# Optimization experiments

Measured on AMD Instinct MI355X. Metric: run time of the kernel, lower is better.

## Reference

```python
import jax, jax.numpy as jnp
import numpy as np

N, M, C, CSKIP, K = 16384, 4096, 256, 128, 3
BIG = 1e10  # distance penalty for cross-batch pairs


def setup_inputs() -> dict:
    key = jax.random.key(0)
    ks = jax.random.split(key, 6)
    return {
        "x": jax.random.normal(ks[0], (M, C), jnp.float32),
        "pos": jax.random.normal(ks[1], (M, 3), jnp.float32),
        "batch": jnp.zeros((M,), jnp.int32),
        "x_skip": jax.random.normal(ks[2], (N, CSKIP), jnp.float32),
        "pos_skip": jax.random.normal(ks[3], (N, 3), jnp.float32),
        "batch_skip": jnp.zeros((N,), jnp.int32),
        "W1": jax.random.normal(ks[4], (C + CSKIP, 256), jnp.float32) * (1.0 / np.sqrt(C + CSKIP)),
        "b1": jnp.zeros((256,), jnp.float32),
        "W2": jax.random.normal(ks[5], (256, 256), jnp.float32) * (1.0 / np.sqrt(256)),
        "b2": jnp.zeros((256,), jnp.float32),
    }


def _knn_idx(pos, pos_skip, batch, batch_skip, k):
    # Squared distances via GEMM form: [N, M]
    a2 = jnp.sum(pos_skip * pos_skip, axis=-1, keepdims=True)      # [N,1]
    b2 = jnp.sum(pos * pos, axis=-1)[None, :]                       # [1,M]
    d2 = a2 + b2 - 2.0 * (pos_skip @ pos.T)                         # [N,M]
    d2 = jnp.where(batch_skip[:, None] != batch[None, :], BIG, d2)
    _, idx = jax.lax.top_k(-d2, k)                                  # [N,k]
    return idx


def reference(x, pos, batch, x_skip, pos_skip, batch_skip, W1, b1, W2, b2):
    idx = _knn_idx(pos, pos_skip, batch, batch_skip, K)             # [N,k] coarse neighbor ids
    # Exact squared dist recomputed from gathered positions (matches torch diff path)
    diff = pos_skip[:, None, :] - pos[idx]                          # [N,k,3]
    d2 = jnp.sum(diff * diff, axis=-1, keepdims=True)               # [N,k,1]
    w = 1.0 / (d2 + 1e-8)                                           # inverse-distance weights
    wsum = jnp.sum(w, axis=1, keepdims=True)                        # per-row scatter_add == sum over k
    w = w / (wsum + 1e-8)
    x_interp = jnp.sum(w * x[idx], axis=1)                          # [N,C]
    h = jnp.concatenate([x_interp, x_skip], axis=1)                 # [N,C+C']
    h = jax.nn.relu(h @ W1 + b1)
    h = jax.nn.relu(h @ W2 + b2)
    return h
```

## Files before the change

kernel.cpp:

```cpp
#include <hip/hip_runtime.h>

typedef float     f4   __attribute__((ext_vector_type(4)));
typedef float     f32x4 __attribute__((ext_vector_type(4)));
typedef _Float16  h8   __attribute__((ext_vector_type(8)));
typedef _Float16  h4   __attribute__((ext_vector_type(4)));
typedef int       i4   __attribute__((ext_vector_type(4)));

#define NQ   16384
#define MP   4096
#define CF   256
#define CSK  128
#define K1   384
#define HID  256

__global__ __launch_bounds__(256) void wconv_kernel(
    const float* __restrict__ W1, const float* __restrict__ W2,
    _Float16* __restrict__ Wt1, _Float16* __restrict__ Wt2)
{
    const int i = blockIdx.x * 256 + threadIdx.x;
    if (i < K1 * HID) {
        const int k = i >> 8, n = i & 255;
        Wt1[(size_t)(k >> 5) * 8192 + ((k >> 3) & 3) * 2048 + n * 8 + (k & 7)]
            = (_Float16)W1[i];
    } else {
        const int i2 = i - K1 * HID;
        const int k = i2 >> 8, n = i2 & 255;
        Wt2[(size_t)(k >> 5) * 8192 + ((k >> 3) & 3) * 2048 + n * 8 + (k & 7)]
            = (_Float16)W2[i2];
    }
}

__global__ __launch_bounds__(256, 2) void fused_kernel(
    const float* __restrict__ pos,
    const float* __restrict__ pos_skip,
    const float* __restrict__ x,
    const float* __restrict__ x_skip,
    const _Float16* __restrict__ Wt1,
    const _Float16* __restrict__ Wt2,
    const float* __restrict__ b1,
    const float* __restrict__ b2,
    float* __restrict__ out)
{
    __shared__ __align__(16) char smem[53760];
    float* px = (float*)smem;
    float* py = (float*)(smem + 16384);
    float* pz = (float*)(smem + 32768);
    unsigned short (*ci)[48]    = (unsigned short (*)[48])(smem + 49152);
    unsigned short (*ci2)[8][3] = (unsigned short (*)[8][3])(smem + 52224);
    int   (*fidx)[3] = (int (*)[3])(smem + 49152);
    float (*fw)[3]   = (float (*)[3])(smem + 49536);
    _Float16 (*As)[392] = (_Float16 (*)[392])smem;
    _Float16 (*Hs)[264] = (_Float16 (*)[264])smem;

    const int tid = threadIdx.x;

    for (int j = tid; j < MP; j += 256) {
        px[j] = pos[3*j+0];
        py[j] = pos[3*j+1];
        pz[j] = pos[3*j+2];
    }
    __syncthreads();

    const int lane = tid & 63;
    const int wv   = tid >> 6;

    {
        float qx[8], qy[8], qz[8];
        #pragma unroll
        for (int k = 0; k < 8; k++) {
            const int q = blockIdx.x * 32 + wv * 8 + k;
            qx[k] = pos_skip[3*q+0];
            qy[k] = pos_skip[3*q+1];
            qz[k] = pos_skip[3*q+2];
        }

        unsigned K0[8], K1v[8], K2[8];
        #pragma unroll
        for (int k = 0; k < 8; k++) { K0[k] = ~0u; K1v[k] = ~0u; K2[k] = ~0u; }

        #define EVAL(PX, PY, PZ, J)                                           \
            _Pragma("unroll")                                                 \
            for (int k = 0; k < 8; k++) {                                     \
                const float dx = qx[k] - (PX), dy = qy[k] - (PY),             \
                            dz = qz[k] - (PZ);                                \
                const float dd = fmaf(dx, dx, fmaf(dy, dy, dz * dz));         \
                const unsigned key = (__float_as_uint(dd) & 0xFFFFF000u) | (J);\
                const unsigned h0 = max(K0[k], key);                          \
                K0[k] = min(K0[k], key);                                      \
                const unsigned n1 = min(K1v[k], h0);                          \
                const unsigned h1 = max(K1v[k], h0);                          \
                K1v[k] = n1;                                                  \
                K2[k] = min(K2[k], h1);                                       \
            }

        float c0x = px[lane],       c1x = px[lane + 64],
              c2x = px[lane + 128], c3x = px[lane + 192];
        float c0y = py[lane],       c1y = py[lane + 64],
              c2y = py[lane + 128], c3y = py[lane + 192];
        float c0z = pz[lane],       c1z = pz[lane + 64],
              c2z = pz[lane + 128], c3z = pz[lane + 192];

        for (int it = 0; it < 64; it += 4) {
            const unsigned jb = it * 64 + lane;
            const float nx0 = px[jb + 256], nx1 = px[jb + 320],
                        nx2 = px[jb + 384], nx3 = px[jb + 448];
            const float ny0 = py[jb + 256], ny1 = py[jb + 320],
                        ny2 = py[jb + 384], ny3 = py[jb + 448];
            const float nz0 = pz[jb + 256], nz1 = pz[jb + 320],
                        nz2 = pz[jb + 384], nz3 = pz[jb + 448];
            EVAL(c0x, c0y, c0z, jb);
            EVAL(c1x, c1y, c1z, jb + 64);
            EVAL(c2x, c2y, c2z, jb + 128);
            EVAL(c3x, c3y, c3z, jb + 192);
            c0x = nx0; c1x = nx1; c2x = nx2; c3x = nx3;
            c0y = ny0; c1y = ny1; c2y = ny2; c3y = ny3;
            c0z = nz0; c1z = nz1; c2z = nz2; c3z = nz3;
        }
        #undef EVAL

        #pragma unroll
        for (int k = 0; k < 8; k++) {
            unsigned a0 = K0[k], a1 = K1v[k], a2 = K2[k];
            {
                const unsigned b0 = (unsigned)__builtin_amdgcn_ds_swizzle((int)a0, 0x041F);
                const unsigned b1 = (unsigned)__builtin_amdgcn_ds_swizzle((int)a1, 0x041F);
                const unsigned b2 = (unsigned)__builtin_amdgcn_ds_swizzle((int)a2, 0x041F);
                const unsigned m0 = min(a0, b0);
                const unsigned c1 = max(a0, b0);
                const unsigned d0 = min(a1, b1), d1 = max(a1, b1);
                const unsigned m1 = min(c1, d0);
                const unsigned m2 = min(min(max(c1, d0), d1), min(a2, b2));
                a0 = m0; a1 = m1; a2 = m2;
            }
            {
                const unsigned b0 = (unsigned)__builtin_amdgcn_ds_swizzle((int)a0, 0x081F);
                const unsigned b1 = (unsigned)__builtin_amdgcn_ds_swizzle((int)a1, 0x081F);
                const unsigned b2 = (unsigned)__builtin_amdgcn_ds_swizzle((int)a2, 0x081F);
                const unsigned m0 = min(a0, b0);
                const unsigned c1 = max(a0, b0);
                const unsigned d0 = min(a1, b1), d1 = max(a1, b1);
                const unsigned m1 = min(c1, d0);
                const unsigned m2 = min(min(max(c1, d0), d1), min(a2, b2));
                a0 = m0; a1 = m1; a2 = m2;
            }
            if (!(lane & 3)) {
                const int q = wv * 8 + k;
                const int pr = lane >> 2;
                ci[q][pr*3+0] = (unsigned short)(a0 & 0xFFFu);
                ci[q][pr*3+1] = (unsigned short)(a1 & 0xFFFu);
                ci[q][pr*3+2] = (unsigned short)(a2 & 0xFFFu);
            }
        }
    }
    __syncthreads();

    {
        const int q    = tid >> 3;
        const int part = tid & 7;
        const int g    = blockIdx.x * 32 + q;
        const double qxd = (double)pos_skip[3*g+0];
        const double qyd = (double)pos_skip[3*g+1];
        const double qzd = (double)pos_skip[3*g+2];
        const double a2d = qxd*qxd + qyd*qyd + qzd*qzd;

        double e0 = 1e300, e1 = 1e300, e2 = 1e300;
        int    j0 = 0,     j1 = 0,     j2 = 0;
        #pragma unroll
        for (int c = 0; c < 6; c++) {
            const int j = ci[q][part*6 + c];
            const double pxd = (double)px[j], pyd = (double)py[j],
                         pzd = (double)pz[j];
            const double b2  = pxd*pxd + pyd*pyd + pzd*pzd;
            const double dot = qxd*pxd + qyd*pyd + qzd*pzd;
            const double d   = (a2d + b2) - 2.0 * dot;
            if (d < e2) {
                if (d < e1) {
                    e2 = e1; j2 = j1;
                    if (d < e0) { e1 = e0; j1 = j0; e0 = d; j0 = j; }
                    else        { e1 = d;  j1 = j; }
                } else { e2 = d; j2 = j; }
            }
        }
        ci2[q][part][0] = (unsigned short)j0;
        ci2[q][part][1] = (unsigned short)j1;
        ci2[q][part][2] = (unsigned short)j2;
    }
    __syncthreads();

    if (tid < 32) {
        const int g = blockIdx.x * 32 + tid;
        const double qxd = (double)pos_skip[3*g+0];
        const double qyd = (double)pos_skip[3*g+1];
        const double qzd = (double)pos_skip[3*g+2];
        const double a2d = qxd*qxd + qyd*qyd + qzd*qzd;

        double e0 = 1e300, e1 = 1e300, e2 = 1e300;
        int    j0 = 0,     j1 = 0,     j2 = 0;
        for (int p = 0; p < 8; p++) {
            #pragma unroll
            for (int s = 0; s < 3; s++) {
                const int j = ci2[tid][p][s];
                const double pxd = (double)px[j], pyd = (double)py[j],
                             pzd = (double)pz[j];
                const double b2  = pxd*pxd + pyd*pyd + pzd*pzd;
                const double dot = qxd*pxd + qyd*pyd + qzd*pzd;
                const double d   = (a2d + b2) - 2.0 * dot;
                if (d < e2) {
                    if (d < e1) {
                        e2 = e1; j2 = j1;
                        if (d < e0) { e1 = e0; j1 = j0; e0 = d; j0 = j; }
                        else        { e1 = d;  j1 = j; }
                    } else { e2 = d; j2 = j; }
                }
            }
        }
        const float sx = pos_skip[3*g+0], sy = pos_skip[3*g+1], sz = pos_skip[3*g+2];
        const int jj[3] = { j0, j1, j2 };
        float wv3[3];
        #pragma unroll
        for (int k = 0; k < 3; k++) {
            const float dx = sx - px[jj[k]], dy = sy - py[jj[k]],
                        dz = sz - pz[jj[k]];
            const float dd = dx*dx + dy*dy + dz*dz;
            wv3[k] = 1.0f / (dd + 1e-8f);
        }
        const float inv = 1.0f / (wv3[0] + wv3[1] + wv3[2] + 1e-8f);
        #pragma unroll
        for (int k = 0; k < 3; k++) {
            fidx[tid][k] = jj[k];
            fw[tid][k]   = wv3[k] * inv;
        }
    }
    __syncthreads();

    const int row0 = blockIdx.x * 32;

    {
        const int r   = tid >> 3;
        const int sub = tid & 7;
        const int j0 = fidx[r][0], j1 = fidx[r][1], j2 = fidx[r][2];
        const float w0 = fw[r][0], w1 = fw[r][1], w2 = fw[r][2];
        const f4* xa = (const f4*)(x + (size_t)j0 * CF);
        const f4* xb = (const f4*)(x + (size_t)j1 * CF);
        const f4* xc = (const f4*)(x + (size_t)j2 * CF);
        const f4* xs = (const f4*)(x_skip + (size_t)(row0 + r) * CSK);
        #pragma unroll
        for (int t = 0; t < 8; t++) {
            const int c4 = t * 8 + sub;
            const f4 a = xa[c4], b = xb[c4], c = xc[c4];
            const f4 v = a * w0 + b * w1 + c * w2;
            h4 hv; hv[0]=(_Float16)v[0]; hv[1]=(_Float16)v[1];
                   hv[2]=(_Float16)v[2]; hv[3]=(_Float16)v[3];
            *(h4*)&As[r][c4 * 4] = hv;
        }
        #pragma unroll
        for (int t = 0; t < 4; t++) {
            const int c4 = t * 8 + sub;
            const f4 v = xs[c4];
            h4 hv; hv[0]=(_Float16)v[0]; hv[1]=(_Float16)v[1];
                   hv[2]=(_Float16)v[2]; hv[3]=(_Float16)v[3];
            *(h4*)&As[r][CF + c4 * 4] = hv;
        }
    }

    const int ln   = tid & 15;
    const int quad = (tid >> 4) & 3;
    const int nb   = wv * 64;
    const int q8   = quad * 8;

    const _Float16* w1b = Wt1 + quad * 2048 + (size_t)(nb + ln) * 8;
    const _Float16* w2b = Wt2 + quad * 2048 + (size_t)(nb + ln) * 8;

    f32x4 acc[2][4];
    #pragma unroll
    for (int mt = 0; mt < 2; mt++)
        #pragma unroll
        for (int nt = 0; nt < 4; nt++) acc[mt][nt] = (f32x4)0.0f;

    h8 B[6][4];
    #pragma unroll
    for (int s = 0; s < 6; s++)
        #pragma unroll
        for (int nt = 0; nt < 4; nt++)
            B[s][nt] = *(const h8*)(w1b + (size_t)s * 8192 + nt * 128);

    __syncthreads();

    #pragma unroll
    for (int kb = 0; kb < 12; kb++) {
        const int s = kb % 6;
        h8 ha[2];
        #pragma unroll
        for (int mt = 0; mt < 2; mt++)
            ha[mt] = *(const h8*)&As[mt*16 + ln][kb*32 + q8];
        h8 hb[4];
        #pragma unroll
        for (int nt = 0; nt < 4; nt++) hb[nt] = B[s][nt];
        if (kb < 6) {
            #pragma unroll
            for (int nt = 0; nt < 4; nt++)
                B[s][nt] = *(const h8*)(w1b + (size_t)(kb+6) * 8192 + nt * 128);
        } else {
            #pragma unroll
            for (int nt = 0; nt < 4; nt++)
                B[s][nt] = *(const h8*)(w2b + (size_t)(kb-6) * 8192 + nt * 128);
        }
        #pragma unroll
        for (int mt = 0; mt < 2; mt++)
            #pragma unroll
            for (int nt = 0; nt < 4; nt++)
                acc[mt][nt] = __builtin_amdgcn_mfma_f32_16x16x32_f16(
                    ha[mt], hb[nt], acc[mt][nt], 0, 0, 0);
    }
    __syncthreads();

    #pragma unroll
    for (int nt = 0; nt < 4; nt++) {
        const int n = nb + nt*16 + ln;
        const float bv = b1[n];
        #pragma unroll
        for (int mt = 0; mt < 2; mt++) {
            #pragma unroll
            for (int r = 0; r < 4; r++) {
                const int m = mt*16 + quad*4 + r;
                Hs[m][n] = (_Float16)fmaxf(acc[mt][nt][r] + bv, 0.0f);
            }
            acc[mt][nt] = (f32x4)0.0f;
        }
    }
    __syncthreads();

    #pragma unroll
    for (int kb = 0; kb < 8; kb++) {
        const int s = kb % 6;
        h8 ha[2];
        #pragma unroll
        for (int mt = 0; mt < 2; mt++)
            ha[mt] = *(const h8*)&Hs[mt*16 + ln][kb*32 + q8];
        h8 hb[4];
        #pragma unroll
        for (int nt = 0; nt < 4; nt++) hb[nt] = B[s][nt];
        if (kb < 2) {
            #pragma unroll
            for (int nt = 0; nt < 4; nt++)
                B[s][nt] = *(const h8*)(w2b + (size_t)(kb+6) * 8192 + nt * 128);
        }
        #pragma unroll
        for (int mt = 0; mt < 2; mt++)
            #pragma unroll
            for (int nt = 0; nt < 4; nt++)
                acc[mt][nt] = __builtin_amdgcn_mfma_f32_16x16x32_f16(
                    ha[mt], hb[nt], acc[mt][nt], 0, 0, 0);
    }

    #pragma unroll
    for (int nt = 0; nt < 4; nt++) {
        const int n = nb + nt*16 + ln;
        const float bv = b2[n];
        #pragma unroll
        for (int mt = 0; mt < 2; mt++)
            #pragma unroll
            for (int r = 0; r < 4; r++) {
                const int m = mt*16 + quad*4 + r;
                out[(size_t)(row0 + m) * HID + n] = fmaxf(acc[mt][nt][r] + bv, 0.0f);
            }
    }
}

extern "C" void kernel_launch(void* const* d_in, const int* in_sizes, int n_in,
                              void* d_out, int out_size, void* d_ws, size_t ws_size,
                              hipStream_t stream) {
    const float* x         = (const float*)d_in[0];
    const float* pos       = (const float*)d_in[1];
    const float* x_skip    = (const float*)d_in[3];
    const float* pos_skip  = (const float*)d_in[4];
    const float* W1        = (const float*)d_in[6];
    const float* b1        = (const float*)d_in[7];
    const float* W2        = (const float*)d_in[8];
    const float* b2        = (const float*)d_in[9];
    float* out = (float*)d_out;

    char* ws = (char*)d_ws;
    _Float16* Wt1 = (_Float16*)ws;
    _Float16* Wt2 = (_Float16*)(ws + 196608);

    wconv_kernel<<<(K1*HID + HID*HID) / 256, 256, 0, stream>>>(W1, W2, Wt1, Wt2);
    fused_kernel<<<NQ / 32, 256, 0, stream>>>(pos, pos_skip, x, x_skip,
                                              Wt1, Wt2, b1, b2, out);
}
```

Baseline: 121.6 us.

## Halve queries per block to 16 and raise occupancy to three blocks

Each block now handles 16 query points instead of 32, which doubles the grid. The per-wave KNN register state, the gather mapping and the MFMA M-tiling shrink to match, and launch bounds now ask for three blocks per CU. The smaller shared buffers let more blocks fit per CU. The trade-off is that every block still loads all 4096 positions into LDS and streams the full weight matrices, so that per-query overhead doubles and weight reuse per block halves.

```diff
diff --git a/kernel.cpp b/kernel.cpp
--- a/kernel.cpp
+++ b/kernel.cpp
@@ -12,6 +12,7 @@
 #define CSK  128
 #define K1   384
 #define HID  256
+#define QB   16
 
 __global__ __launch_bounds__(256) void wconv_kernel(
     const float* __restrict__ W1, const float* __restrict__ W2,
@@ -30,7 +31,7 @@
     }
 }
 
-__global__ __launch_bounds__(256, 2) void fused_kernel(
+__global__ __launch_bounds__(256, 3) void fused_kernel(
     const float* __restrict__ pos,
     const float* __restrict__ pos_skip,
     const float* __restrict__ x,
@@ -41,14 +42,14 @@
     const float* __restrict__ b2,
     float* __restrict__ out)
 {
-    __shared__ __align__(16) char smem[53760];
+    __shared__ __align__(16) char smem[51456];
     float* px = (float*)smem;
     float* py = (float*)(smem + 16384);
     float* pz = (float*)(smem + 32768);
     unsigned short (*ci)[48]    = (unsigned short (*)[48])(smem + 49152);
-    unsigned short (*ci2)[8][3] = (unsigned short (*)[8][3])(smem + 52224);
+    unsigned short (*ci2)[8][3] = (unsigned short (*)[8][3])(smem + 50688);
     int   (*fidx)[3] = (int (*)[3])(smem + 49152);
-    float (*fw)[3]   = (float (*)[3])(smem + 49536);
+    float (*fw)[3]   = (float (*)[3])(smem + 49344);
     _Float16 (*As)[392] = (_Float16 (*)[392])smem;
     _Float16 (*Hs)[264] = (_Float16 (*)[264])smem;
 
@@ -65,22 +66,22 @@
     const int wv   = tid >> 6;
 
     {
-        float qx[8], qy[8], qz[8];
-        #pragma unroll
-        for (int k = 0; k < 8; k++) {
-            const int q = blockIdx.x * 32 + wv * 8 + k;
+        float qx[4], qy[4], qz[4];
+        #pragma unroll
+        for (int k = 0; k < 4; k++) {
+            const int q = blockIdx.x * QB + wv * 4 + k;
             qx[k] = pos_skip[3*q+0];
             qy[k] = pos_skip[3*q+1];
             qz[k] = pos_skip[3*q+2];
         }
 
-        unsigned K0[8], K1v[8], K2[8];
-        #pragma unroll
-        for (int k = 0; k < 8; k++) { K0[k] = ~0u; K1v[k] = ~0u; K2[k] = ~0u; }
+        unsigned K0[4], K1v[4], K2[4];
+        #pragma unroll
+        for (int k = 0; k < 4; k++) { K0[k] = ~0u; K1v[k] = ~0u; K2[k] = ~0u; }
 
         #define EVAL(PX, PY, PZ, J)                                           \
             _Pragma("unroll")                                                 \
-            for (int k = 0; k < 8; k++) {                                     \
+            for (int k = 0; k < 4; k++) {                                     \
                 const float dx = qx[k] - (PX), dy = qy[k] - (PY),             \
                             dz = qz[k] - (PZ);                                \
                 const float dd = fmaf(dx, dx, fmaf(dy, dy, dz * dz));         \
@@ -119,7 +120,7 @@
         #undef EVAL
 
         #pragma unroll
-        for (int k = 0; k < 8; k++) {
+        for (int k = 0; k < 4; k++) {
             unsigned a0 = K0[k], a1 = K1v[k], a2 = K2[k];
             {
                 const unsigned b0 = (unsigned)__builtin_amdgcn_ds_swizzle((int)a0, 0x041F);
@@ -144,7 +145,7 @@
                 a0 = m0; a1 = m1; a2 = m2;
             }
             if (!(lane & 3)) {
-                const int q = wv * 8 + k;
+                const int q = wv * 4 + k;
                 const int pr = lane >> 2;
                 ci[q][pr*3+0] = (unsigned short)(a0 & 0xFFFu);
                 ci[q][pr*3+1] = (unsigned short)(a1 & 0xFFFu);
@@ -154,10 +155,10 @@
     }
     __syncthreads();
 
-    {
+    if (tid < 8 * QB) {
         const int q    = tid >> 3;
         const int part = tid & 7;
-        const int g    = blockIdx.x * 32 + q;
+        const int g    = blockIdx.x * QB + q;
         const double qxd = (double)pos_skip[3*g+0];
         const double qyd = (double)pos_skip[3*g+1];
         const double qzd = (double)pos_skip[3*g+2];
@@ -187,8 +188,8 @@
     }
     __syncthreads();
 
-    if (tid < 32) {
-        const int g = blockIdx.x * 32 + tid;
+    if (tid < QB) {
+        const int g = blockIdx.x * QB + tid;
         const double qxd = (double)pos_skip[3*g+0];
         const double qyd = (double)pos_skip[3*g+1];
         const double qzd = (double)pos_skip[3*g+2];
@@ -233,11 +234,11 @@
     }
     __syncthreads();
 
-    const int row0 = blockIdx.x * 32;
+    const int row0 = blockIdx.x * QB;
 
     {
-        const int r   = tid >> 3;
-        const int sub = tid & 7;
+        const int r   = tid >> 4;
+        const int sub = tid & 15;
         const int j0 = fidx[r][0], j1 = fidx[r][1], j2 = fidx[r][2];
         const float w0 = fw[r][0], w1 = fw[r][1], w2 = fw[r][2];
         const f4* xa = (const f4*)(x + (size_t)j0 * CF);
@@ -245,8 +246,8 @@
         const f4* xc = (const f4*)(x + (size_t)j2 * CF);
         const f4* xs = (const f4*)(x_skip + (size_t)(row0 + r) * CSK);
         #pragma unroll
-        for (int t = 0; t < 8; t++) {
-            const int c4 = t * 8 + sub;
+        for (int t = 0; t < 4; t++) {
+            const int c4 = t * 16 + sub;
             const f4 a = xa[c4], b = xb[c4], c = xc[c4];
             const f4 v = a * w0 + b * w1 + c * w2;
             h4 hv; hv[0]=(_Float16)v[0]; hv[1]=(_Float16)v[1];
@@ -254,8 +255,8 @@
             *(h4*)&As[r][c4 * 4] = hv;
         }
         #pragma unroll
-        for (int t = 0; t < 4; t++) {
-            const int c4 = t * 8 + sub;
+        for (int t = 0; t < 2; t++) {
+            const int c4 = t * 16 + sub;
             const f4 v = xs[c4];
             h4 hv; hv[0]=(_Float16)v[0]; hv[1]=(_Float16)v[1];
                    hv[2]=(_Float16)v[2]; hv[3]=(_Float16)v[3];
@@ -271,11 +272,9 @@
     const _Float16* w1b = Wt1 + quad * 2048 + (size_t)(nb + ln) * 8;
     const _Float16* w2b = Wt2 + quad * 2048 + (size_t)(nb + ln) * 8;
 
-    f32x4 acc[2][4];
-    #pragma unroll
-    for (int mt = 0; mt < 2; mt++)
-        #pragma unroll
-        for (int nt = 0; nt < 4; nt++) acc[mt][nt] = (f32x4)0.0f;
+    f32x4 acc[4];
+    #pragma unroll
+    for (int nt = 0; nt < 4; nt++) acc[nt] = (f32x4)0.0f;
 
     h8 B[6][4];
     #pragma unroll
@@ -289,10 +288,7 @@
     #pragma unroll
     for (int kb = 0; kb < 12; kb++) {
         const int s = kb % 6;
-        h8 ha[2];
-        #pragma unroll
-        for (int mt = 0; mt < 2; mt++)
-            ha[mt] = *(const h8*)&As[mt*16 + ln][kb*32 + q8];
+        const h8 ha = *(const h8*)&As[ln][kb*32 + q8];
         h8 hb[4];
         #pragma unroll
         for (int nt = 0; nt < 4; nt++) hb[nt] = B[s][nt];
@@ -306,11 +302,8 @@
                 B[s][nt] = *(const h8*)(w2b + (size_t)(kb-6) * 8192 + nt * 128);
         }
         #pragma unroll
-        for (int mt = 0; mt < 2; mt++)
-            #pragma unroll
-            for (int nt = 0; nt < 4; nt++)
-                acc[mt][nt] = __builtin_amdgcn_mfma_f32_16x16x32_f16(
-                    ha[mt], hb[nt], acc[mt][nt], 0, 0, 0);
+        for (int nt = 0; nt < 4; nt++)
+            acc[nt] = __builtin_amdgcn_mfma_f32_16x16x32_f16(ha, hb[nt], acc[nt], 0, 0, 0);
     }
     __syncthreads();
 
@@ -319,24 +312,18 @@
         const int n = nb + nt*16 + ln;
         const float bv = b1[n];
         #pragma unroll
-        for (int mt = 0; mt < 2; mt++) {
-            #pragma unroll
-            for (int r = 0; r < 4; r++) {
-                const int m = mt*16 + quad*4 + r;
-                Hs[m][n] = (_Float16)fmaxf(acc[mt][nt][r] + bv, 0.0f);
-            }
-            acc[mt][nt] = (f32x4)0.0f;
-        }
+        for (int r = 0; r < 4; r++) {
+            const int m = quad*4 + r;
+            Hs[m][n] = (_Float16)fmaxf(acc[nt][r] + bv, 0.0f);
+        }
+        acc[nt] = (f32x4)0.0f;
     }
     __syncthreads();
 
     #pragma unroll
     for (int kb = 0; kb < 8; kb++) {
         const int s = kb % 6;
-        h8 ha[2];
-        #pragma unroll
-        for (int mt = 0; mt < 2; mt++)
-            ha[mt] = *(const h8*)&Hs[mt*16 + ln][kb*32 + q8];
+        const h8 ha = *(const h8*)&Hs[ln][kb*32 + q8];
         h8 hb[4];
         #pragma unroll
         for (int nt = 0; nt < 4; nt++) hb[nt] = B[s][nt];
@@ -346,11 +333,8 @@
                 B[s][nt] = *(const h8*)(w2b + (size_t)(kb+6) * 8192 + nt * 128);
         }
         #pragma unroll
-        for (int mt = 0; mt < 2; mt++)
-            #pragma unroll
-            for (int nt = 0; nt < 4; nt++)
-                acc[mt][nt] = __builtin_amdgcn_mfma_f32_16x16x32_f16(
-                    ha[mt], hb[nt], acc[mt][nt], 0, 0, 0);
+        for (int nt = 0; nt < 4; nt++)
+            acc[nt] = __builtin_amdgcn_mfma_f32_16x16x32_f16(ha, hb[nt], acc[nt], 0, 0, 0);
     }
 
     #pragma unroll
@@ -358,12 +342,10 @@
         const int n = nb + nt*16 + ln;
         const float bv = b2[n];
         #pragma unroll
-        for (int mt = 0; mt < 2; mt++)
-            #pragma unroll
-            for (int r = 0; r < 4; r++) {
-                const int m = mt*16 + quad*4 + r;
-                out[(size_t)(row0 + m) * HID + n] = fmaxf(acc[mt][nt][r] + bv, 0.0f);
-            }
+        for (int r = 0; r < 4; r++) {
+            const int m = quad*4 + r;
+            out[(size_t)(row0 + m) * HID + n] = fmaxf(acc[nt][r] + bv, 0.0f);
+        }
     }
 }
 
@@ -385,6 +367,6 @@
     _Float16* Wt2 = (_Float16*)(ws + 196608);
 
     wconv_kernel<<<(K1*HID + HID*HID) / 256, 256, 0, stream>>>(W1, W2, Wt1, Wt2);
-    fused_kernel<<<NQ / 32, 256, 0, stream>>>(pos, pos_skip, x, x_skip,
+    fused_kernel<<<NQ / QB, 256, 0, stream>>>(pos, pos_skip, x, x_skip,
                                               Wt1, Wt2, b1, b2, out);
 }
```

After: 119.3 us. About the same (-1.9%).
